# Kernel tuning notes

Measured on AMD Instinct MI355X. Metric: run time of the kernel, lower is better.

## Reference

```python
import jax, jax.numpy as jnp
import numpy as np

N_NODES = 100000


def setup_inputs() -> dict:
    key = jax.random.key(0)
    ks = jax.random.split(key, 6)
    F_IN, F_CH, F_OUT = 64, 64, 64
    E = 1200000
    x = jax.random.normal(ks[0], (N_NODES, F_IN), dtype=jnp.float32)
    edge_index = jax.random.randint(ks[1], (2, E), 0, N_NODES, dtype=jnp.int64)
    # MLP params (PyTorch Linear default init scale ~ 1/sqrt(fan_in))
    s1 = 1.0 / np.sqrt(2 * F_IN)
    s2 = 1.0 / np.sqrt(F_CH)
    W1 = jax.random.uniform(ks[2], (2 * F_IN, F_CH), jnp.float32, -s1, s1)
    b1 = jax.random.uniform(ks[3], (F_CH,), jnp.float32, -s1, s1)
    W2 = jax.random.uniform(ks[4], (F_CH, F_OUT), jnp.float32, -s2, s2)
    b2 = jax.random.uniform(ks[5], (F_OUT,), jnp.float32, -s2, s2)
    return {"x": x, "edge_index": edge_index, "W1": W1, "b1": b1, "W2": W2, "b2": b2}


def reference(x, edge_index, W1, b1, W2, b2):
    # PyG EdgeConv with aggr='add': out_i = sum_j MLP(concat[x_i, x_j - x_i])
    src = edge_index[0]  # j (source / neighbor)
    dst = edge_index[1]  # i (target, aggregation index)
    x_i = x[dst]                     # [E, F]
    x_j = x[src]                     # [E, F]
    msg = jnp.concatenate([x_i, x_j - x_i], axis=-1)      # [E, 2F]
    h = jax.nn.relu(msg @ W1 + b1) @ W2 + b2               # [E, F_out]
    agg = jax.ops.segment_sum(h, dst, num_segments=N_NODES)  # [N, F_out]
    return jnp.tanh(agg)
```

## Files before the change

kernel.cpp:

```cpp
#include <hip/hip_runtime.h>
#include <math.h>


#define FDIM 64
#define BN 64
#define BSH 6
#define CAPB 1024
#define MAXB 2048
#define EPB 4096
#define PRE_SMEM 16384

typedef unsigned int u32;
typedef unsigned short u16;
typedef _Float16 hf;
typedef _Float16 h2 __attribute__((ext_vector_type(2)));

__device__ __forceinline__ u32 f2h(float f) {
    union { u16 s; hf h; } c; c.h = (hf)f; return (u32)c.s;
}
__device__ __forceinline__ h2 u2h2(u32 u) {
    union { u32 u; h2 h; } c; c.u = u; return c.h;
}

__global__ __launch_bounds__(256) void prep_k(
    const float* __restrict__ x, const float* __restrict__ W1,
    u16* __restrict__ Bmh, const int* __restrict__ ei,
    u32* __restrict__ slotB, int* __restrict__ gcnt,
    int N, int E, int NB, int nPre, int nBin)
{
    __shared__ __align__(16) char smem[PRE_SMEM];
    const int idx = blockIdx.x;
    const int tid = threadIdx.x;

    if ((idx % 6) == 5) {
        const int bb = idx / 6;
        if (bb >= nBin) return;
        int* histL = (int*)smem;
        int* gbase = histL + MAXB;
        const int e0 = bb * EPB;

        for (int j = tid; j < NB; j += 256) histL[j] = 0;
        __syncthreads();

        #pragma unroll 8
        for (int i = 0; i < EPB / 256; ++i) {
            int e = e0 + i * 256 + tid;
            if (e < E) {
                int d = ei[E + e];
                atomicAdd(&histL[d >> BSH], 1);
            }
        }
        __syncthreads();

        for (int j = tid; j < NB; j += 256) {
            int h = histL[j];
            gbase[j] = (h > 0) ? atomicAdd(&gcnt[j], h) : 0;
            histL[j] = 0;
        }
        __syncthreads();

        #pragma unroll 8
        for (int i = 0; i < EPB / 256; ++i) {
            int e = e0 + i * 256 + tid;
            if (e < E) {
                int s = ei[e];
                int d = ei[E + e];
                int b = d >> BSH;
                int pos = gbase[b] + atomicAdd(&histL[b], 1);
                if (pos < CAPB)
                    slotB[(size_t)b * CAPB + pos] =
                        ((u32)(d & (BN - 1)) << 20) | (u32)s;
            }
        }
        return;
    }

    const int pb = idx - idx / 6;
    if (pb >= nPre) return;
    u32 (*Wch)[64] = (u32(*)[64])smem;
    u32* xs = (u32*)(smem + 8192);

    const int node0 = pb * 64;

    for (int i = tid; i < 2048; i += 256) {
        int kk = i >> 6, c = i & 63;
        float a0 = W1[(64 + 2 * kk) * 64 + c];
        float a1 = W1[(64 + 2 * kk + 1) * 64 + c];
        ((u32*)smem)[i] = f2h(a0) | (f2h(a1) << 16);
    }
    {
        const float4* X4 = (const float4*)x;
        #pragma unroll
        for (int it = 0; it < 4; ++it) {
            int i = it * 256 + tid;
            int n = i >> 4, k4 = i & 15;
            int gn = node0 + n;
            float4 v = make_float4(0.f, 0.f, 0.f, 0.f);
            if (gn < N) v = X4[(size_t)gn * 16 + k4];
            int r0 = 2 * k4, r1 = r0 + 1;
            int g = n >> 2, lo = n & 3;
            xs[r0 * 64 + (((g ^ (r0 & 15)) << 2) | lo)] = f2h(v.x) | (f2h(v.y) << 16);
            xs[r1 * 64 + (((g ^ (r1 & 15)) << 2) | lo)] = f2h(v.z) | (f2h(v.w) << 16);
        }
    }
    __syncthreads();

    const int ng = tid & 15, cg = tid >> 4;
    const int n0 = ng * 4, c0 = cg * 4;

    float acc[4][4];
    #pragma unroll
    for (int ni = 0; ni < 4; ++ni)
        #pragma unroll
        for (int ci = 0; ci < 4; ++ci) acc[ni][ci] = 0.f;

    #pragma unroll 4
    for (int kk = 0; kk < 32; ++kk) {
        uint4 xq = *(const uint4*)&xs[kk * 64 + ((ng ^ (kk & 15)) << 2)];
        uint4 w = *(const uint4*)&Wch[kk][c0];
        h2 wv[4] = {u2h2(w.x), u2h2(w.y), u2h2(w.z), u2h2(w.w)};
        u32 xq4[4] = {xq.x, xq.y, xq.z, xq.w};
        #pragma unroll
        for (int ni = 0; ni < 4; ++ni) {
            h2 xh = u2h2(xq4[ni]);
            #pragma unroll
            for (int ci = 0; ci < 4; ++ci)
                acc[ni][ci] = __builtin_amdgcn_fdot2(xh, wv[ci], acc[ni][ci], false);
        }
    }

    #pragma unroll
    for (int ni = 0; ni < 4; ++ni) {
        int n = node0 + n0 + ni;
        if (n >= N) break;
        uint2 pk;
        pk.x = f2h(acc[ni][0]) | (f2h(acc[ni][1]) << 16);
        pk.y = f2h(acc[ni][2]) | (f2h(acc[ni][3]) << 16);
        *(uint2*)&Bmh[(size_t)n * 64 + c0] = pk;
    }
}

__global__ __launch_bounds__(256) void fused_agg(
    const float* __restrict__ x, const float* __restrict__ W1,
    const float* __restrict__ b1, const u16* __restrict__ Bmh,
    const u32* __restrict__ slotB, const int* __restrict__ gcnt,
    const float* __restrict__ W2, const float* __restrict__ b2,
    float* __restrict__ out, int N)
{
    __shared__ __align__(16) char uni[16896];
    __shared__ int histL[BN];
    __shared__ int rowO[BN + 1];
    __shared__ int ofs[BN];
    __shared__ float b2s[64];
    __shared__ float b1s[64];

    u32 (*Wdh)[64] = (u32(*)[64])uni;
    u32* xs = (u32*)(uni + 8192);
    uint2* aggTb = (uint2*)uni;
    u32* csrS = (u32*)(uni + 8704);
    u32* eStage = (u32*)(uni + 12800);
    u32* W2kp = (u32*)(uni + 8704);

    const int tid = threadIdx.x;
    const int b = blockIdx.x;
    const int node0 = b * BN;
    const int cntB = min(gcnt[b], CAPB);

    for (int i = tid; i < 2048; i += 256) {
        int kk = i >> 6, c = i & 63;
        int k0 = 2 * kk, k1 = k0 + 1;
        float a0 = W1[k0 * 64 + c] - W1[(64 + k0) * 64 + c];
        float a1 = W1[k1 * 64 + c] - W1[(64 + k1) * 64 + c];
        ((u32*)uni)[i] = f2h(a0) | (f2h(a1) << 16);
    }
    {
        const float4* X4 = (const float4*)x;
        #pragma unroll
        for (int it = 0; it < 4; ++it) {
            int i = it * 256 + tid;
            int n = i >> 4, k4 = i & 15;
            int gn = node0 + n;
            float4 v = make_float4(0.f, 0.f, 0.f, 0.f);
            if (gn < N) v = X4[(size_t)gn * 16 + k4];
            int r0 = 2 * k4, r1 = r0 + 1;
            int g = n >> 2, lo = n & 3;
            xs[r0 * 64 + (((g ^ (r0 & 15)) << 2) | lo)] = f2h(v.x) | (f2h(v.y) << 16);
            xs[r1 * 64 + (((g ^ (r1 & 15)) << 2) | lo)] = f2h(v.z) | (f2h(v.w) << 16);
        }
    }
    if (tid < 64) { b2s[tid] = b2[tid]; b1s[tid] = b1[tid]; }
    if (tid < BN) histL[tid] = 0;
    __syncthreads();

    const int q = tid & 15, ng = tid >> 4;
    const int q4 = q * 4;
    float af[4][4];
    #pragma unroll
    for (int h = 0; h < 4; ++h)
        #pragma unroll
        for (int ci = 0; ci < 4; ++ci) af[h][ci] = b1s[q4 + ci];

    #pragma unroll 4
    for (int kk = 0; kk < 32; ++kk) {
        uint4 xq = *(const uint4*)&xs[kk * 64 + ((ng ^ (kk & 15)) << 2)];
        uint4 wq = *(const uint4*)&Wdh[kk][q4];
        h2 wv[4] = {u2h2(wq.x), u2h2(wq.y), u2h2(wq.z), u2h2(wq.w)};
        u32 xq4[4] = {xq.x, xq.y, xq.z, xq.w};
        #pragma unroll
        for (int h = 0; h < 4; ++h) {
            h2 xh = u2h2(xq4[h]);
            #pragma unroll
            for (int ci = 0; ci < 4; ++ci)
                af[h][ci] = __builtin_amdgcn_fdot2(xh, wv[ci], af[h][ci], false);
        }
    }
    u32 pa[4][2];
    #pragma unroll
    for (int h = 0; h < 4; ++h) {
        pa[h][0] = f2h(af[h][0]) | (f2h(af[h][1]) << 16);
        pa[h][1] = f2h(af[h][2]) | (f2h(af[h][3]) << 16);
    }
    __syncthreads();

    for (int i = tid; i < cntB; i += 256) {
        u32 e = slotB[(size_t)b * CAPB + i];
        eStage[i] = e;
        atomicAdd(&histL[e >> 20], 1);
    }
    __syncthreads();

    if (tid < 32) {
        int l = tid;
        int h0 = histL[2 * l], h1 = histL[2 * l + 1];
        int s = h0 + h1, inc = s;
        #pragma unroll
        for (int off = 1; off < 32; off <<= 1) {
            int t = __shfl_up(inc, off);
            if (l >= off) inc += t;
        }
        int base = inc - s;
        rowO[2 * l] = base; rowO[2 * l + 1] = base + h0;
        ofs[2 * l] = base;  ofs[2 * l + 1] = base + h0;
        if (l == 31) rowO[BN] = inc;
    }
    __syncthreads();

    for (int i = tid; i < cntB; i += 256) {
        u32 e = eStage[i];
        int pos = atomicAdd(&ofs[e >> 20], 1);
        csrS[pos] = e & 0xFFFFFu;
    }
    __syncthreads();

    {
        const uint2* __restrict__ B2 = (const uint2*)Bmh;
        const h2 SEL10 = {(_Float16)1.f, (_Float16)0.f};
        const h2 SEL01 = {(_Float16)0.f, (_Float16)1.f};
        const h2 HZ = {(_Float16)0.f, (_Float16)0.f};
        #pragma unroll
        for (int h = 0; h < 4; ++h) {
            int nl = ng * 4 + h;
            int gn = node0 + nl;
            int start = rowO[nl];
            int d = (gn < N) ? (rowO[nl + 1] - start) : 0;
            h2 A0 = u2h2(pa[h][0]), A1 = u2h2(pa[h][1]);
            float ac0 = 0.f, ac1 = 0.f, ac2 = 0.f, ac3 = 0.f;

            int j = 0;
            for (; j + 8 <= d; j += 8) {
                int ss[8];
                uint2 bb[8];
                #pragma unroll
                for (int t = 0; t < 8; ++t) ss[t] = csrS[start + j + t];
                #pragma unroll
                for (int t = 0; t < 8; ++t) bb[t] = B2[(size_t)ss[t] * 16 + q];
                #pragma unroll
                for (int t = 0; t < 8; ++t) {
                    h2 t0 = A0 + u2h2(bb[t].x);
                    h2 t1 = A1 + u2h2(bb[t].y);
                    t0 = __builtin_elementwise_max(t0, HZ);
                    t1 = __builtin_elementwise_max(t1, HZ);
                    ac0 = __builtin_amdgcn_fdot2(t0, SEL10, ac0, false);
                    ac1 = __builtin_amdgcn_fdot2(t0, SEL01, ac1, false);
                    ac2 = __builtin_amdgcn_fdot2(t1, SEL10, ac2, false);
                    ac3 = __builtin_amdgcn_fdot2(t1, SEL01, ac3, false);
                }
            }
            if (j < d) {
                int ss[8];
                uint2 bb[8];
                #pragma unroll
                for (int t = 0; t < 8; ++t) ss[t] = csrS[start + min(j + t, d - 1)];
                #pragma unroll
                for (int t = 0; t < 8; ++t) bb[t] = B2[(size_t)ss[t] * 16 + q];
                #pragma unroll
                for (int t = 0; t < 8; ++t) {
                    if (j + t >= d) { bb[t].x = 0xFC00FC00u; bb[t].y = 0xFC00FC00u; }
                    h2 t0 = A0 + u2h2(bb[t].x);
                    h2 t1 = A1 + u2h2(bb[t].y);
                    t0 = __builtin_elementwise_max(t0, HZ);
                    t1 = __builtin_elementwise_max(t1, HZ);
                    ac0 = __builtin_amdgcn_fdot2(t0, SEL10, ac0, false);
                    ac1 = __builtin_amdgcn_fdot2(t0, SEL01, ac1, false);
                    ac2 = __builtin_amdgcn_fdot2(t1, SEL10, ac2, false);
                    ac3 = __builtin_amdgcn_fdot2(t1, SEL01, ac3, false);
                }
            }
            uint2 pk;
            pk.x = f2h(ac0) | (f2h(ac1) << 16);
            pk.y = f2h(ac2) | (f2h(ac3) << 16);
            aggTb[nl * 17 + q] = pk;
        }
    }
    __syncthreads();

    for (int i = tid; i < 2048; i += 256) {
        int kk = i >> 6, c = i & 63;
        W2kp[i] = f2h(W2[(2 * kk) * 64 + c]) | (f2h(W2[(2 * kk + 1) * 64 + c]) << 16);
    }
    __syncthreads();

    {
        const int cg = tid & 15, g = tid >> 4;
        const int c0 = cg * 4;
        const int nb0 = g * 4;
        float o[4][4];
        #pragma unroll
        for (int ni = 0; ni < 4; ++ni) {
            float dg = (float)(rowO[nb0 + ni + 1] - rowO[nb0 + ni]);
            #pragma unroll
            for (int ci = 0; ci < 4; ++ci) o[ni][ci] = dg * b2s[c0 + ci];
        }
        #pragma unroll 4
        for (int kc = 0; kc < 16; ++kc) {
            uint2 u0 = aggTb[(nb0 + 0) * 17 + kc];
            uint2 u1 = aggTb[(nb0 + 1) * 17 + kc];
            uint2 u2 = aggTb[(nb0 + 2) * 17 + kc];
            uint2 u3 = aggTb[(nb0 + 3) * 17 + kc];
            uint4 wA = *(const uint4*)&W2kp[(2 * kc) * 64 + c0];
            uint4 wB = *(const uint4*)&W2kp[(2 * kc + 1) * 64 + c0];
            h2 wa[4] = {u2h2(wA.x), u2h2(wA.y), u2h2(wA.z), u2h2(wA.w)};
            h2 wb[4] = {u2h2(wB.x), u2h2(wB.y), u2h2(wB.z), u2h2(wB.w)};
            h2 a0x = u2h2(u0.x), a0y = u2h2(u0.y);
            h2 a1x = u2h2(u1.x), a1y = u2h2(u1.y);
            h2 a2x = u2h2(u2.x), a2y = u2h2(u2.y);
            h2 a3x = u2h2(u3.x), a3y = u2h2(u3.y);
            #pragma unroll
            for (int ci = 0; ci < 4; ++ci) {
                o[0][ci] = __builtin_amdgcn_fdot2(a0x, wa[ci], o[0][ci], false);
                o[0][ci] = __builtin_amdgcn_fdot2(a0y, wb[ci], o[0][ci], false);
                o[1][ci] = __builtin_amdgcn_fdot2(a1x, wa[ci], o[1][ci], false);
                o[1][ci] = __builtin_amdgcn_fdot2(a1y, wb[ci], o[1][ci], false);
                o[2][ci] = __builtin_amdgcn_fdot2(a2x, wa[ci], o[2][ci], false);
                o[2][ci] = __builtin_amdgcn_fdot2(a2y, wb[ci], o[2][ci], false);
                o[3][ci] = __builtin_amdgcn_fdot2(a3x, wa[ci], o[3][ci], false);
                o[3][ci] = __builtin_amdgcn_fdot2(a3y, wb[ci], o[3][ci], false);
            }
        }
        #pragma unroll
        for (int ni = 0; ni < 4; ++ni) {
            int gn = node0 + nb0 + ni;
            if (gn < N) {
                float4 r = make_float4(tanhf(o[ni][0]), tanhf(o[ni][1]),
                                       tanhf(o[ni][2]), tanhf(o[ni][3]));
                ((float4*)out)[(size_t)gn * 16 + cg] = r;
            }
        }
    }
}

extern "C" void kernel_launch(void* const* d_in, const int* in_sizes, int n_in,
                              void* d_out, int out_size, void* d_ws, size_t ws_size,
                              hipStream_t stream)
{
    const float* x  = (const float*)d_in[0];
    const int*   ei = (const int*)d_in[1];
    const float* W1 = (const float*)d_in[2];
    const float* b1 = (const float*)d_in[3];
    const float* W2 = (const float*)d_in[4];
    const float* b2 = (const float*)d_in[5];
    float* out = (float*)d_out;

    const int N = in_sizes[0] / FDIM;
    const int E = in_sizes[1] / 2;
    const int NB = (N + BN - 1) / BN;

    u16*   Bmh   = (u16*)d_ws;
    u32*   slotB = (u32*)(Bmh + (size_t)N * FDIM);
    int*   gcnt  = (int*)(slotB + (size_t)NB * CAPB);

    hipMemsetAsync(gcnt, 0, (size_t)NB * sizeof(int), stream);

    const int nPre = (N + 63) / 64;
    const int nBin = (E + EPB - 1) / EPB;
    int T = (nPre * 6 + 4) / 5;
    while (T - T / 6 < nPre) ++T;
    if (T < 6 * nBin) T = 6 * nBin;

    prep_k<<<T, 256, 0, stream>>>(x, W1, Bmh, ei, slotB, gcnt,
                                  N, E, NB, nPre, nBin);
    fused_agg<<<NB, 256, 0, stream>>>(x, W1, b1, Bmh, slotB, gcnt, W2, b2, out, N);
}
```

Baseline: 169.7 us.

## Move per-node A-side projection into prep kernel and store it in workspace

```diff
diff --git a/kernel.cpp b/kernel.cpp
--- a/kernel.cpp
+++ b/kernel.cpp
@@ -8,7 +8,7 @@
 #define CAPB 1024
 #define MAXB 2048
 #define EPB 4096
-#define PRE_SMEM 16384
+#define PRE_SMEM 24576
 
 typedef unsigned int u32;
 typedef unsigned short u16;
@@ -24,6 +24,7 @@
 
 __global__ __launch_bounds__(256) void prep_k(
     const float* __restrict__ x, const float* __restrict__ W1,
+    const float* __restrict__ b1, u16* __restrict__ Ah,
     u16* __restrict__ Bmh, const int* __restrict__ ei,
     u32* __restrict__ slotB, int* __restrict__ gcnt,
     int N, int E, int NB, int nPre, int nBin)
@@ -77,16 +78,24 @@
 
     const int pb = idx - idx / 6;
     if (pb >= nPre) return;
-    u32 (*Wch)[64] = (u32(*)[64])smem;
-    u32* xs = (u32*)(smem + 8192);
+    u32 (*Wch)[128] = (u32(*)[128])smem;
+    u32* xs = (u32*)(smem + 16384);
 
     const int node0 = pb * 64;
 
-    for (int i = tid; i < 2048; i += 256) {
-        int kk = i >> 6, c = i & 63;
-        float a0 = W1[(64 + 2 * kk) * 64 + c];
-        float a1 = W1[(64 + 2 * kk + 1) * 64 + c];
-        ((u32*)smem)[i] = f2h(a0) | (f2h(a1) << 16);
+    for (int i = tid; i < 4096; i += 256) {
+        int kk = i >> 7, c = i & 127;
+        int k0 = 2 * kk, k1 = k0 + 1;
+        float a0, a1;
+        if (c < 64) {
+            a0 = W1[k0 * 64 + c] - W1[(64 + k0) * 64 + c];
+            a1 = W1[k1 * 64 + c] - W1[(64 + k1) * 64 + c];
+        } else {
+            int cc = c - 64;
+            a0 = W1[(64 + k0) * 64 + cc];
+            a1 = W1[(64 + k1) * 64 + cc];
+        }
+        Wch[kk][c] = f2h(a0) | (f2h(a1) << 16);
     }
     {
         const float4* X4 = (const float4*)x;
@@ -106,25 +115,29 @@
     __syncthreads();
 
     const int ng = tid & 15, cg = tid >> 4;
-    const int n0 = ng * 4, c0 = cg * 4;
-
-    float acc[4][4];
+    const int n0 = ng * 4, c0 = cg * 8;
+
+    float acc[4][8];
     #pragma unroll
-    for (int ni = 0; ni < 4; ++ni)
-        #pragma unroll
-        for (int ci = 0; ci < 4; ++ci) acc[ni][ci] = 0.f;
+    for (int ci = 0; ci < 8; ++ci) {
+        float init = (c0 < 64) ? b1[c0 + ci] : 0.f;
+        #pragma unroll
+        for (int ni = 0; ni < 4; ++ni) acc[ni][ci] = init;
+    }
 
     #pragma unroll 4
     for (int kk = 0; kk < 32; ++kk) {
         uint4 xq = *(const uint4*)&xs[kk * 64 + ((ng ^ (kk & 15)) << 2)];
-        uint4 w = *(const uint4*)&Wch[kk][c0];
-        h2 wv[4] = {u2h2(w.x), u2h2(w.y), u2h2(w.z), u2h2(w.w)};
+        uint4 w0 = *(const uint4*)&Wch[kk][c0];
+        uint4 w1 = *(const uint4*)&Wch[kk][c0 + 4];
+        h2 wv[8] = {u2h2(w0.x), u2h2(w0.y), u2h2(w0.z), u2h2(w0.w),
+                    u2h2(w1.x), u2h2(w1.y), u2h2(w1.z), u2h2(w1.w)};
         u32 xq4[4] = {xq.x, xq.y, xq.z, xq.w};
         #pragma unroll
         for (int ni = 0; ni < 4; ++ni) {
             h2 xh = u2h2(xq4[ni]);
             #pragma unroll
-            for (int ci = 0; ci < 4; ++ci)
+            for (int ci = 0; ci < 8; ++ci)
                 acc[ni][ci] = __builtin_amdgcn_fdot2(xh, wv[ci], acc[ni][ci], false);
         }
     }
@@ -133,16 +146,18 @@
     for (int ni = 0; ni < 4; ++ni) {
         int n = node0 + n0 + ni;
         if (n >= N) break;
-        uint2 pk;
+        uint4 pk;
         pk.x = f2h(acc[ni][0]) | (f2h(acc[ni][1]) << 16);
         pk.y = f2h(acc[ni][2]) | (f2h(acc[ni][3]) << 16);
-        *(uint2*)&Bmh[(size_t)n * 64 + c0] = pk;
+        pk.z = f2h(acc[ni][4]) | (f2h(acc[ni][5]) << 16);
+        pk.w = f2h(acc[ni][6]) | (f2h(acc[ni][7]) << 16);
+        if (c0 < 64) *(uint4*)&Ah[(size_t)n * 64 + c0] = pk;
+        else         *(uint4*)&Bmh[(size_t)n * 64 + (c0 - 64)] = pk;
     }
 }
 
 __global__ __launch_bounds__(256) void fused_agg(
-    const float* __restrict__ x, const float* __restrict__ W1,
-    const float* __restrict__ b1, const u16* __restrict__ Bmh,
+    const u16* __restrict__ Ah, const u16* __restrict__ Bmh,
     const u32* __restrict__ slotB, const int* __restrict__ gcnt,
     const float* __restrict__ W2, const float* __restrict__ b2,
     float* __restrict__ out, int N)
@@ -152,10 +167,7 @@
     __shared__ int rowO[BN + 1];
     __shared__ int ofs[BN];
     __shared__ float b2s[64];
-    __shared__ float b1s[64];
-
-    u32 (*Wdh)[64] = (u32(*)[64])uni;
-    u32* xs = (u32*)(uni + 8192);
+
     uint2* aggTb = (uint2*)uni;
     u32* csrS = (u32*)(uni + 8704);
     u32* eStage = (u32*)(uni + 12800);
@@ -166,60 +178,8 @@
     const int node0 = b * BN;
     const int cntB = min(gcnt[b], CAPB);
 
-    for (int i = tid; i < 2048; i += 256) {
-        int kk = i >> 6, c = i & 63;
-        int k0 = 2 * kk, k1 = k0 + 1;
-        float a0 = W1[k0 * 64 + c] - W1[(64 + k0) * 64 + c];
-        float a1 = W1[k1 * 64 + c] - W1[(64 + k1) * 64 + c];
-        ((u32*)uni)[i] = f2h(a0) | (f2h(a1) << 16);
-    }
-    {
-        const float4* X4 = (const float4*)x;
-        #pragma unroll
-        for (int it = 0; it < 4; ++it) {
-            int i = it * 256 + tid;
-            int n = i >> 4, k4 = i & 15;
-            int gn = node0 + n;
-            float4 v = make_float4(0.f, 0.f, 0.f, 0.f);
-            if (gn < N) v = X4[(size_t)gn * 16 + k4];
-            int r0 = 2 * k4, r1 = r0 + 1;
-            int g = n >> 2, lo = n & 3;
-            xs[r0 * 64 + (((g ^ (r0 & 15)) << 2) | lo)] = f2h(v.x) | (f2h(v.y) << 16);
-            xs[r1 * 64 + (((g ^ (r1 & 15)) << 2) | lo)] = f2h(v.z) | (f2h(v.w) << 16);
-        }
-    }
-    if (tid < 64) { b2s[tid] = b2[tid]; b1s[tid] = b1[tid]; }
+    if (tid < 64) b2s[tid] = b2[tid];
     if (tid < BN) histL[tid] = 0;
-    __syncthreads();
-
-    const int q = tid & 15, ng = tid >> 4;
-    const int q4 = q * 4;
-    float af[4][4];
-    #pragma unroll
-    for (int h = 0; h < 4; ++h)
-        #pragma unroll
-        for (int ci = 0; ci < 4; ++ci) af[h][ci] = b1s[q4 + ci];
-
-    #pragma unroll 4
-    for (int kk = 0; kk < 32; ++kk) {
-        uint4 xq = *(const uint4*)&xs[kk * 64 + ((ng ^ (kk & 15)) << 2)];
-        uint4 wq = *(const uint4*)&Wdh[kk][q4];
-        h2 wv[4] = {u2h2(wq.x), u2h2(wq.y), u2h2(wq.z), u2h2(wq.w)};
-        u32 xq4[4] = {xq.x, xq.y, xq.z, xq.w};
-        #pragma unroll
-        for (int h = 0; h < 4; ++h) {
-            h2 xh = u2h2(xq4[h]);
-            #pragma unroll
-            for (int ci = 0; ci < 4; ++ci)
-                af[h][ci] = __builtin_amdgcn_fdot2(xh, wv[ci], af[h][ci], false);
-        }
-    }
-    u32 pa[4][2];
-    #pragma unroll
-    for (int h = 0; h < 4; ++h) {
-        pa[h][0] = f2h(af[h][0]) | (f2h(af[h][1]) << 16);
-        pa[h][1] = f2h(af[h][2]) | (f2h(af[h][3]) << 16);
-    }
     __syncthreads();
 
     for (int i = tid; i < cntB; i += 256) {
@@ -252,8 +212,10 @@
     }
     __syncthreads();
 
+    const int q = tid & 15, ng = tid >> 4;
     {
         const uint2* __restrict__ B2 = (const uint2*)Bmh;
+        const uint2* __restrict__ A2 = (const uint2*)Ah;
         const h2 SEL10 = {(_Float16)1.f, (_Float16)0.f};
         const h2 SEL01 = {(_Float16)0.f, (_Float16)1.f};
         const h2 HZ = {(_Float16)0.f, (_Float16)0.f};
@@ -263,7 +225,9 @@
             int gn = node0 + nl;
             int start = rowO[nl];
             int d = (gn < N) ? (rowO[nl + 1] - start) : 0;
-            h2 A0 = u2h2(pa[h][0]), A1 = u2h2(pa[h][1]);
+            uint2 ua = make_uint2(0u, 0u);
+            if (gn < N) ua = A2[(size_t)gn * 16 + q];
+            h2 A0 = u2h2(ua.x), A1 = u2h2(ua.y);
             float ac0 = 0.f, ac1 = 0.f, ac2 = 0.f, ac3 = 0.f;
 
             int j = 0;
@@ -385,7 +349,8 @@
     const int E = in_sizes[1] / 2;
     const int NB = (N + BN - 1) / BN;
 
-    u16*   Bmh   = (u16*)d_ws;
+    u16*   Ah    = (u16*)d_ws;
+    u16*   Bmh   = Ah + (size_t)N * FDIM;
     u32*   slotB = (u32*)(Bmh + (size_t)N * FDIM);
     int*   gcnt  = (int*)(slotB + (size_t)NB * CAPB);
 
@@ -397,7 +362,7 @@
     while (T - T / 6 < nPre) ++T;
     if (T < 6 * nBin) T = 6 * nBin;
 
-    prep_k<<<T, 256, 0, stream>>>(x, W1, Bmh, ei, slotB, gcnt,
+    prep_k<<<T, 256, 0, stream>>>(x, W1, b1, Ah, Bmh, ei, slotB, gcnt,
                                   N, E, NB, nPre, nBin);
-    fused_agg<<<NB, 256, 0, stream>>>(x, W1, b1, Bmh, slotB, gcnt, W2, b2, out, N);
-}
+    fused_agg<<<NB, 256, 0, stream>>>(Ah, Bmh, slotB, gcnt, W2, b2, out, N);
+}
```

Result: faster. 166.2 us (-2.0%).
